# Kernel optimization log

Hardware: AMD Instinct MI355X
Metric: run time of the kernel (lower is better)

## Reference

```python
import jax, jax.numpy as jnp
import numpy as np

VOCAB = 32000
FEAT = 1024
B, T = 16, 256


def setup_inputs() -> dict:
    key = jax.random.key(0)
    ks = jax.random.split(key, 12)
    s_in = 1.0 / np.sqrt(FEAT)
    inp = {
        "x": jax.random.randint(ks[0], (B, T), 0, VOCAB),
        "h0": jnp.zeros((2, B, FEAT), jnp.float32),
        "emb": jax.random.normal(ks[1], (VOCAB, FEAT), jnp.float32) * 0.02,
        "W_ih0": jax.random.uniform(ks[2], (3 * FEAT, FEAT), jnp.float32, -s_in, s_in),
        "W_hh0": jax.random.uniform(ks[3], (3 * FEAT, FEAT), jnp.float32, -s_in, s_in),
        "b_ih0": jax.random.uniform(ks[4], (3 * FEAT,), jnp.float32, -s_in, s_in),
        "b_hh0": jax.random.uniform(ks[5], (3 * FEAT,), jnp.float32, -s_in, s_in),
        "W_ih1": jax.random.uniform(ks[6], (3 * FEAT, FEAT), jnp.float32, -s_in, s_in),
        "W_hh1": jax.random.uniform(ks[7], (3 * FEAT, FEAT), jnp.float32, -s_in, s_in),
        "b_ih1": jax.random.uniform(ks[8], (3 * FEAT,), jnp.float32, -s_in, s_in),
        "b_hh1": jax.random.uniform(ks[9], (3 * FEAT,), jnp.float32, -s_in, s_in),
        "dec_b": jnp.zeros((VOCAB,), jnp.float32),
    }
    return inp


def _gru_layer(xs, h0, W_ih, W_hh, b_ih, b_hh):
    # xs: [T, B, H_in]; h0: [B, H]. PyTorch gate order: r, z, n.
    x_proj = jnp.einsum('tbi,gi->tbg', xs, W_ih) + b_ih  # [T, B, 3H]

    def step(h, xp):
        hp = h @ W_hh.T + b_hh  # [B, 3H]
        xr, xz, xn = jnp.split(xp, 3, axis=-1)
        hr, hz, hn = jnp.split(hp, 3, axis=-1)
        r = jax.nn.sigmoid(xr + hr)
        z = jax.nn.sigmoid(xz + hz)
        n = jnp.tanh(xn + r * hn)
        h_new = (1.0 - z) * n + z * h
        return h_new, h_new

    h_last, ys = jax.lax.scan(step, h0, x_proj)
    return ys, h_last


def reference(x, h0, emb, W_ih0, W_hh0, b_ih0, b_hh0, W_ih1, W_hh1, b_ih1, b_hh1, dec_b):
    xs = emb[x]  # [B, T, H]
    xs = jnp.transpose(xs, (1, 0, 2))  # time-major [T, B, H]
    ys0, h_last0 = _gru_layer(xs, h0[0], W_ih0, W_hh0, b_ih0, b_hh0)
    ys1, h_last1 = _gru_layer(ys0, h0[1], W_ih1, W_hh1, b_ih1, b_hh1)
    out = jnp.transpose(ys1, (1, 0, 2))  # [B, T, H]
    logits = jnp.einsum('bth,vh->btv', out, emb) + dec_b  # tied decoder
    hidden = jnp.stack([h_last0, h_last1], axis=0)  # [2, B, H]
    return logits, hidden
```

## Files before the change

### kernel.cpp

```cpp
#include <hip/hip_runtime.h>
#include <math.h>

#define FEAT 1024
#define NB 16
#define NT 256
#define VOCAB 32000
#define G3 3072
#define NWG 256
#define FLAG_STRIDE 32
#define NGRP 8
#define GSZ 32
#define NXPT 24

#define BK 32
#define LDH 40
#define SMEM_BYTES 75584

typedef float f4 __attribute__((ext_vector_type(4)));
typedef float f32x4 __attribute__((ext_vector_type(4)));
typedef _Float16 half4v __attribute__((ext_vector_type(4)));
typedef _Float16 half8v __attribute__((ext_vector_type(8)));

__global__ __launch_bounds__(256) void gather_kernel(const int* __restrict__ x,
                                                     const float* __restrict__ emb,
                                                     float* __restrict__ xs) {
    int row = blockIdx.x;
    int t = row >> 4;
    int b = row & 15;
    int tok = x[b * NT + t];
    const float4* src = (const float4*)(emb + (size_t)tok * FEAT);
    float4* dst = (float4*)(xs + (size_t)row * FEAT);
    dst[threadIdx.x] = src[threadIdx.x];
}

__device__ __forceinline__ void store_f32_sc(float* p, float v) {
    asm volatile("global_store_dword %0, %1, off sc0 sc1" :: "v"(p), "v"(v) : "memory");
}
__device__ __forceinline__ void bar_arrive(unsigned* flag, unsigned expected) {
    asm volatile("s_waitcnt vmcnt(0)\n\t"
                 "global_store_dword %0, %1, off sc0 sc1"
                 :: "v"(flag), "v"(expected) : "memory");
}
__device__ __forceinline__ void bar_poll(const unsigned* p, unsigned expected) {
    unsigned v; int spins = 0;
    while (true) {
        asm volatile("global_load_dword %0, %1, off sc0 sc1\n\t"
                     "s_waitcnt vmcnt(0)"
                     : "=&v"(v) : "v"(p) : "memory");
        if (v >= expected) break;
        if (++spins > (1 << 20)) break;
        __builtin_amdgcn_s_sleep(1);
    }
}

__device__ __forceinline__ void gemm_tile(char* smemraw,
        const float* __restrict__ A, const float* __restrict__ Bm,
        const float* __restrict__ bias, float* __restrict__ C,
        int N, int K, int m_t, int n_t, int perm,
        int coherent, unsigned* cnt) {
    _Float16* AhS = (_Float16*)smemraw;
    _Float16* AlS = AhS + 128 * LDH;
    _Float16* BhS = AlS + 128 * LDH;
    _Float16* BlS = BhS + 128 * LDH;

    int tid = threadIdx.x;
    int srow = tid >> 1;
    int shf = tid & 1;

    const float* aptr = A + (size_t)(m_t * 128 + srow) * K + shf * 16;
    const float* bptr = Bm + (size_t)(n_t * 128 + srow) * K + shf * 16;

    int wid = tid >> 6;
    int wr = wid >> 1, wc = wid & 1;
    int lane = tid & 63;
    int fr = lane & 15;
    int ke = lane >> 4;

    f32x4 acc[4][4];
#pragma unroll
    for (int i = 0; i < 4; i++)
#pragma unroll
        for (int j = 0; j < 4; j++) acc[i][j] = (f32x4){0.f, 0.f, 0.f, 0.f};

    float4 a4[4], b4[4];
#pragma unroll
    for (int q = 0; q < 4; q++) {
        a4[q] = *(const float4*)(aptr + q * 4);
        b4[q] = *(const float4*)(bptr + q * 4);
    }

    for (int k0 = 0; k0 < K; k0 += BK) {
        __syncthreads();
#pragma unroll
        for (int q = 0; q < 4; q++) {
            half4v hh, hl;
            hh.x = (_Float16)a4[q].x; hl.x = (_Float16)(a4[q].x - (float)hh.x);
            hh.y = (_Float16)a4[q].y; hl.y = (_Float16)(a4[q].y - (float)hh.y);
            hh.z = (_Float16)a4[q].z; hl.z = (_Float16)(a4[q].z - (float)hh.z);
            hh.w = (_Float16)a4[q].w; hl.w = (_Float16)(a4[q].w - (float)hh.w);
            int o = srow * LDH + shf * 16 + q * 4;
            *(half4v*)&AhS[o] = hh;
            *(half4v*)&AlS[o] = hl;
            half4v gh, gl;
            gh.x = (_Float16)b4[q].x; gl.x = (_Float16)(b4[q].x - (float)gh.x);
            gh.y = (_Float16)b4[q].y; gl.y = (_Float16)(b4[q].y - (float)gh.y);
            gh.z = (_Float16)b4[q].z; gl.z = (_Float16)(b4[q].z - (float)gh.z);
            gh.w = (_Float16)b4[q].w; gl.w = (_Float16)(b4[q].w - (float)gh.w);
            *(half4v*)&BhS[o] = gh;
            *(half4v*)&BlS[o] = gl;
        }
        __syncthreads();

        if (k0 + BK < K) {
#pragma unroll
            for (int q = 0; q < 4; q++) {
                a4[q] = *(const float4*)(aptr + k0 + BK + q * 4);
                b4[q] = *(const float4*)(bptr + k0 + BK + q * 4);
            }
        }

        half8v ah[4], al[4], bh[4], bl[4];
#pragma unroll
        for (int i = 0; i < 4; i++) {
            int ao = (wr * 64 + i * 16 + fr) * LDH + ke * 8;
            ah[i] = *(const half8v*)&AhS[ao];
            al[i] = *(const half8v*)&AlS[ao];
            int bo = (wc * 64 + i * 16 + fr) * LDH + ke * 8;
            bh[i] = *(const half8v*)&BhS[bo];
            bl[i] = *(const half8v*)&BlS[bo];
        }
#pragma unroll
        for (int i = 0; i < 4; i++)
#pragma unroll
            for (int j = 0; j < 4; j++) {
                acc[i][j] = __builtin_amdgcn_mfma_f32_16x16x32_f16(ah[i], bh[j], acc[i][j], 0, 0, 0);
                acc[i][j] = __builtin_amdgcn_mfma_f32_16x16x32_f16(ah[i], bl[j], acc[i][j], 0, 0, 0);
                acc[i][j] = __builtin_amdgcn_mfma_f32_16x16x32_f16(al[i], bh[j], acc[i][j], 0, 0, 0);
            }
    }

#pragma unroll
    for (int j = 0; j < 4; j++) {
        int col = n_t * 128 + wc * 64 + j * 16 + fr;
        float bv = bias[col];
#pragma unroll
        for (int i = 0; i < 4; i++) {
#pragma unroll
            for (int v = 0; v < 4; v++) {
                int mrow = m_t * 128 + wr * 64 + i * 16 + 4 * ke + v;
                int orow = perm ? (((mrow & 15) << 8) | (mrow >> 4)) : mrow;
                float val = acc[i][j][v] + bv;
                if (coherent) store_f32_sc(&C[(size_t)orow * N + col], val);
                else          C[(size_t)orow * N + col] = val;
            }
        }
    }
    if (cnt) {
        asm volatile("s_waitcnt vmcnt(0)" ::: "memory");
        __syncthreads();
        if (tid == 0)
            __hip_atomic_fetch_add(cnt, 1u, __ATOMIC_RELAXED, __HIP_MEMORY_SCOPE_AGENT);
    }
}

__device__ __forceinline__ void scan_layer(char* smemraw,
        const float* __restrict__ xp, const float* __restrict__ Whh,
        const float* __restrict__ bhh, const float* __restrict__ h0src,
        float* __restrict__ ys, float* __restrict__ hid,
        unsigned* __restrict__ flags, unsigned* __restrict__ gflags,
        const unsigned* __restrict__ xpcnt) {
    float* w_lds   = (float*)smemraw;
    float* red     = w_lds + 12 * 1024;
    float* sums    = red + 192 * 33;
    float* bhh_lds = sums + 256;

    __builtin_amdgcn_s_setprio(1);

    int wg = blockIdx.x;
    int j0 = wg * 4;
    int tid = threadIdx.x;

    for (int rr = 0; rr < 12; rr++) {
        int gate = rr >> 2, jloc = rr & 3;
        int grow = gate * FEAT + j0 + jloc;
        float4 v = ((const float4*)(Whh + (size_t)grow * FEAT))[tid];
        *(float4*)(w_lds + rr * 1024 + tid * 4) = v;
    }
    if (tid < 12) {
        int gate = tid >> 2, jloc = tid & 3;
        bhh_lds[tid] = bhh[gate * FEAT + j0 + jloc];
    }
    if (xpcnt && tid == 0) bar_poll(&xpcnt[0], NXPT);
    __syncthreads();

    int bg = tid >> 6;
    int kc = tid & 63;
    int pb = tid >> 2, pjl = tid & 3, pj = j0 + pjl;

    float hreg = 0.f;
    if (tid < 64) hreg = h0src[pb * FEAT + pj];

    for (int t = 0; t < NT; t++) {
        float xr = 0.f, xz = 0.f, xnv = 0.f;
        if (tid < 64) {
            const float* xpr = xp + (size_t)(t * NB + pb) * G3;
            xr = xpr[pj]; xz = xpr[FEAT + pj]; xnv = xpr[2 * FEAT + pj];
        }

        const float* hc = (t == 0) ? h0src : (ys + (size_t)(t - 1) * NB * FEAT);
        f4 h4[16];
#pragma unroll
        for (int bi = 0; bi < 4; bi++) {
            const float* hp = hc + (size_t)(bg * 4 + bi) * FEAT + kc * 4;
#pragma unroll
            for (int q = 0; q < 4; q++)
                h4[bi * 4 + q] = *(const f4*)(hp + q * 256);
        }

        float part[48];
#pragma unroll
        for (int i = 0; i < 48; i++) part[i] = 0.f;
#pragma unroll
        for (int q = 0; q < 4; q++) {
            int kof = q * 256 + kc * 4;
#pragma unroll
            for (int rr = 0; rr < 12; rr++) {
                f4 w = *(const f4*)&w_lds[rr * 1024 + kof];
#pragma unroll
                for (int bi = 0; bi < 4; bi++) {
                    f4 h = h4[bi * 4 + q];
                    float p = part[rr * 4 + bi];
                    p = fmaf(h.x, w.x, p); p = fmaf(h.y, w.y, p);
                    p = fmaf(h.z, w.z, p); p = fmaf(h.w, w.w, p);
                    part[rr * 4 + bi] = p;
                }
            }
        }
#pragma unroll
        for (int i = 0; i < 48; i++) part[i] += __shfl_xor(part[i], 1);
        if ((kc & 1) == 0) {
#pragma unroll
            for (int rr = 0; rr < 12; rr++)
#pragma unroll
                for (int bi = 0; bi < 4; bi++)
                    red[(rr * 16 + bg * 4 + bi) * 33 + (kc >> 1)] = part[rr * 4 + bi];
        }
        __syncthreads();

        if (tid < 192) {
            float s = 0.f;
#pragma unroll
            for (int c = 0; c < 32; c++) s += red[tid * 33 + c];
            sums[tid] = s;
        }
        __syncthreads();

        if (tid < 64) {
            float dr = sums[pjl * 16 + pb] + bhh_lds[pjl];
            float dz = sums[(4 + pjl) * 16 + pb] + bhh_lds[4 + pjl];
            float dn = sums[(8 + pjl) * 16 + pb] + bhh_lds[8 + pjl];
            float r = 1.f / (1.f + expf(-(xr + dr)));
            float z = 1.f / (1.f + expf(-(xz + dz)));
            float n = tanhf(xnv + r * dn);
            float hv = (1.f - z) * n + z * hreg;
            hreg = hv;
            store_f32_sc(ys + (size_t)(t * NB + pb) * FEAT + pj, hv);
            if (t == NT - 1) hid[pb * FEAT + pj] = hv;
        }

        unsigned expected = (unsigned)(t + 1);
        __syncthreads();
        if (tid == 0) {
            bar_arrive(&flags[wg * FLAG_STRIDE], expected);
            if (xpcnt) {
                int nx = (t + 1 < NT) ? (t + 1) : (NT - 1);
                bar_poll(&xpcnt[(nx >> 3) * FLAG_STRIDE], NXPT);
            }
        }
        if (wg < NGRP) {
            if (tid < GSZ) bar_poll(flags + (wg * GSZ + tid) * FLAG_STRIDE, expected);
            if (tid == 0) {
                asm volatile("global_store_dword %0, %1, off sc0 sc1"
                             :: "v"(&gflags[wg * FLAG_STRIDE]), "v"(expected) : "memory");
            }
        }
        if (tid < NGRP) bar_poll(gflags + tid * FLAG_STRIDE, expected);
        __builtin_amdgcn_sched_barrier(0);
        __syncthreads();
    }
}

__global__ __launch_bounds__(256, 2) void phase1(
        float* __restrict__ xp, const float* __restrict__ Whh0,
        const float* __restrict__ bhh0, const float* __restrict__ h0,
        float* __restrict__ ys0, float* __restrict__ hid,
        unsigned* __restrict__ flags0, unsigned* __restrict__ gflags0,
        const float* __restrict__ xs,
        const float* __restrict__ Wih0, const float* __restrict__ bih0,
        unsigned* __restrict__ xpcnt,
        const float* __restrict__ Wih1, const float* __restrict__ bih1) {
    __shared__ __align__(16) char smem[SMEM_BYTES];
    int bid = blockIdx.x;
    if (bid < NWG) {
        scan_layer(smem, xp, Whh0, bhh0, h0, ys0, hid, flags0, gflags0, xpcnt);
    } else if (bid < NWG + (4096 / 128) * NXPT) {
        int b2 = bid - NWG;
        int perGroup = 8 * NXPT;
        int g = b2 / perGroup, rix = b2 % perGroup;
        int n_t = rix / 8, m_t = g * 8 + (rix % 8);
        gemm_tile(smem, xs, Wih0, bih0, xp, G3, FEAT, m_t, n_t, 0,
                  1, &xpcnt[m_t * FLAG_STRIDE]);
    } else {
        int b2 = bid - NWG - (4096 / 128) * NXPT;
        int perGroup = 8 * NXPT;
        int g = b2 / perGroup, rix = b2 % perGroup;
        int n_t = rix / 8, m_t = g * 8 + (rix % 8);
        unsigned gate = (unsigned)((m_t + 1) * 8);
        if (threadIdx.x < NGRP) bar_poll(gflags0 + threadIdx.x * FLAG_STRIDE, gate);
        __builtin_amdgcn_sched_barrier(0);
        __syncthreads();
        gemm_tile(smem, ys0, Wih1, bih1, xp, G3, FEAT, m_t, n_t, 0, 0, nullptr);
    }
}

__global__ __launch_bounds__(256, 2) void phase2(
        const float* __restrict__ xp, const float* __restrict__ Whh1,
        const float* __restrict__ bhh1, const float* __restrict__ h0b,
        float* __restrict__ ys1, float* __restrict__ hid1,
        unsigned* __restrict__ flags1, unsigned* __restrict__ gflags1,
        const float* __restrict__ emb, const float* __restrict__ dec_b,
        float* __restrict__ out) {
    __shared__ __align__(16) char smem[SMEM_BYTES];
    if (blockIdx.x < NWG) {
        scan_layer(smem, xp, Whh1, bhh1, h0b, ys1, hid1, flags1, gflags1, nullptr);
    } else {
        int bid = blockIdx.x - NWG;
        int perGroup = 8 * (VOCAB >> 7);
        int g = bid / perGroup, rix = bid % perGroup;
        int n_t = rix / 8, m_t = g * 8 + (rix % 8);
        unsigned gate = (unsigned)((m_t + 1) * 8);
        if (threadIdx.x < NGRP) bar_poll(gflags1 + threadIdx.x * FLAG_STRIDE, gate);
        __builtin_amdgcn_sched_barrier(0);
        __syncthreads();
        gemm_tile(smem, ys1, emb, dec_b, out, VOCAB, FEAT, m_t, n_t, 1, 0, nullptr);
    }
}

extern "C" void kernel_launch(void* const* d_in, const int* in_sizes, int n_in,
                              void* d_out, int out_size, void* d_ws, size_t ws_size,
                              hipStream_t stream) {
    const int*   x     = (const int*)d_in[0];
    const float* h0    = (const float*)d_in[1];
    const float* emb   = (const float*)d_in[2];
    const float* W_ih0 = (const float*)d_in[3];
    const float* W_hh0 = (const float*)d_in[4];
    const float* b_ih0 = (const float*)d_in[5];
    const float* b_hh0 = (const float*)d_in[6];
    const float* W_ih1 = (const float*)d_in[7];
    const float* W_hh1 = (const float*)d_in[8];
    const float* b_ih1 = (const float*)d_in[9];
    const float* b_hh1 = (const float*)d_in[10];
    const float* dec_b = (const float*)d_in[11];

    float* out = (float*)d_out;
    float* hid_out = out + (size_t)NB * NT * VOCAB;

    float* ws  = (float*)d_ws;
    float* xp  = ws;
    float* xs  = xp + (size_t)4096 * 3072;
    float* ys0 = xs + (size_t)4096 * 1024;
    float* pad = ys0 + (size_t)4096 * 1024;
    unsigned* flags0  = (unsigned*)(pad + 2 * NB * FEAT);
    unsigned* gflags0 = flags0 + NWG * FLAG_STRIDE;
    unsigned* flags1  = gflags0 + NGRP * FLAG_STRIDE;
    unsigned* gflags1 = flags1 + NWG * FLAG_STRIDE;
    unsigned* xpcnt   = gflags1 + NGRP * FLAG_STRIDE;
    float* ys1 = xs;

    hipMemsetAsync((void*)flags0, 0,
                   (2 * NWG + 2 * NGRP + 32) * FLAG_STRIDE * sizeof(unsigned),
                   stream);

    gather_kernel<<<dim3(NT * NB), dim3(256), 0, stream>>>(x, emb, xs);

    phase1<<<dim3(NWG + 2 * (4096 / 128) * NXPT), dim3(256), 0, stream>>>(
        xp, W_hh0, b_hh0, h0, ys0, hid_out, flags0, gflags0,
        xs, W_ih0, b_ih0, xpcnt, W_ih1, b_ih1);

    phase2<<<dim3(NWG + (4096 / 128) * (VOCAB / 128)), dim3(256), 0, stream>>>(
        xp, W_hh1, b_hh1, h0 + NB * FEAT, ys1, hid_out + NB * FEAT,
        flags1, gflags1, emb, dec_b, out);
}
```

Before: 3.679 ms.

## Fuse both GRU layer scans into one delayed wavefront chain kernel

```diff
diff --git a/kernel.cpp b/kernel.cpp
--- a/kernel.cpp
+++ b/kernel.cpp
@@ -11,10 +11,12 @@
 #define NGRP 8
 #define GSZ 32
 #define NXPT 24
+#define DLY 32
+#define CHAIN (NT + DLY)
 
 #define BK 32
 #define LDH 40
-#define SMEM_BYTES 75584
+#define SMEM_BYTES 63104
 
 typedef float f4 __attribute__((ext_vector_type(4)));
 typedef float f32x4 __attribute__((ext_vector_type(4)));
@@ -163,16 +165,33 @@
     }
 }
 
-__device__ __forceinline__ void scan_layer(char* smemraw,
-        const float* __restrict__ xp, const float* __restrict__ Whh,
-        const float* __restrict__ bhh, const float* __restrict__ h0src,
-        float* __restrict__ ys, float* __restrict__ hid,
+__global__ __launch_bounds__(256, 2) void gemm_split16(
+        const float* __restrict__ A, const float* __restrict__ Bm,
+        const float* __restrict__ bias, float* __restrict__ C,
+        int N, int K, int GM, int perm) {
+    __shared__ __align__(16) char smem[4 * 128 * LDH * 2];
+    int nNt = N >> 7;
+    int perGroup = GM * nNt;
+    int g = blockIdx.x / perGroup;
+    int rix = blockIdx.x % perGroup;
+    int n_t = rix / GM;
+    int m_t = g * GM + (rix % GM);
+    gemm_tile(smem, A, Bm, bias, C, N, K, m_t, n_t, perm, 0, nullptr);
+}
+
+__device__ __forceinline__ void scan_chain(char* smemraw,
+        float* __restrict__ xp, const float* __restrict__ Whh0,
+        const float* __restrict__ bhh0, const float* __restrict__ Whh1,
+        const float* __restrict__ bhh1, const float* __restrict__ h0all,
+        float* __restrict__ ys0, float* __restrict__ ys1,
+        float* __restrict__ hid,
         unsigned* __restrict__ flags, unsigned* __restrict__ gflags,
-        const unsigned* __restrict__ xpcnt) {
-    float* w_lds   = (float*)smemraw;
-    float* red     = w_lds + 12 * 1024;
-    float* sums    = red + 192 * 33;
-    float* bhh_lds = sums + 256;
+        const unsigned* __restrict__ xpcnt, const unsigned* __restrict__ xp1cnt) {
+    float* w_lds = (float*)smemraw;
+    float* red   = w_lds + 12 * 1024;
+    float* sums  = red + 192 * 17;
+    float* b0l   = sums + 192;
+    float* b1l   = b0l + 12;
 
     __builtin_amdgcn_s_setprio(1);
 
@@ -183,99 +202,222 @@
     for (int rr = 0; rr < 12; rr++) {
         int gate = rr >> 2, jloc = rr & 3;
         int grow = gate * FEAT + j0 + jloc;
-        float4 v = ((const float4*)(Whh + (size_t)grow * FEAT))[tid];
+        float4 v = ((const float4*)(Whh0 + (size_t)grow * FEAT))[tid];
         *(float4*)(w_lds + rr * 1024 + tid * 4) = v;
     }
     if (tid < 12) {
         int gate = tid >> 2, jloc = tid & 3;
-        bhh_lds[tid] = bhh[gate * FEAT + j0 + jloc];
-    }
-    if (xpcnt && tid == 0) bar_poll(&xpcnt[0], NXPT);
+        b0l[tid] = bhh0[gate * FEAT + j0 + jloc];
+        b1l[tid] = bhh1[gate * FEAT + j0 + jloc];
+    }
+    if (tid == 0) bar_poll(&xpcnt[0], NXPT);
     __syncthreads();
 
     int bg = tid >> 6;
     int kc = tid & 63;
     int pb = tid >> 2, pjl = tid & 3, pj = j0 + pjl;
 
-    float hreg = 0.f;
-    if (tid < 64) hreg = h0src[pb * FEAT + pj];
-
-    for (int t = 0; t < NT; t++) {
+    const float* w1g0 = Whh1 + (size_t)j0 * FEAT;
+    const float* w1g1 = Whh1 + (size_t)(FEAT + j0) * FEAT;
+    const float* w1g2 = Whh1 + (size_t)(2 * FEAT + j0) * FEAT;
+
+    float hreg0 = 0.f, hreg1 = 0.f;
+    if (tid < 64) {
+        hreg0 = h0all[pb * FEAT + pj];
+        hreg1 = h0all[NB * FEAT + pb * FEAT + pj];
+    }
+
+    for (int s = 0; s < CHAIN; s++) {
+        int do0 = (s < NT);
+        int t1 = s - DLY;
+        int do1 = (t1 >= 0);
+
         float xr = 0.f, xz = 0.f, xnv = 0.f;
-        if (tid < 64) {
-            const float* xpr = xp + (size_t)(t * NB + pb) * G3;
+        if (do0 && tid < 64) {
+            const float* xpr = xp + (size_t)(s * NB + pb) * G3;
             xr = xpr[pj]; xz = xpr[FEAT + pj]; xnv = xpr[2 * FEAT + pj];
         }
-
-        const float* hc = (t == 0) ? h0src : (ys + (size_t)(t - 1) * NB * FEAT);
-        f4 h4[16];
-#pragma unroll
-        for (int bi = 0; bi < 4; bi++) {
-            const float* hp = hc + (size_t)(bg * 4 + bi) * FEAT + kc * 4;
-#pragma unroll
-            for (int q = 0; q < 4; q++)
-                h4[bi * 4 + q] = *(const f4*)(hp + q * 256);
-        }
-
-        float part[48];
-#pragma unroll
-        for (int i = 0; i < 48; i++) part[i] = 0.f;
-#pragma unroll
-        for (int q = 0; q < 4; q++) {
-            int kof = q * 256 + kc * 4;
-#pragma unroll
-            for (int rr = 0; rr < 12; rr++) {
-                f4 w = *(const f4*)&w_lds[rr * 1024 + kof];
-#pragma unroll
-                for (int bi = 0; bi < 4; bi++) {
-                    f4 h = h4[bi * 4 + q];
-                    float p = part[rr * 4 + bi];
-                    p = fmaf(h.x, w.x, p); p = fmaf(h.y, w.y, p);
-                    p = fmaf(h.z, w.z, p); p = fmaf(h.w, w.w, p);
-                    part[rr * 4 + bi] = p;
+        float x1r, x1z, x1n;
+        if (do1 && tid < 64) {
+            const float* xpr = xp + (size_t)(t1 * NB + pb) * G3;
+            asm volatile(
+                "global_load_dword %0, %3, off sc0 sc1\n\t"
+                "global_load_dword %1, %4, off sc0 sc1\n\t"
+                "global_load_dword %2, %5, off sc0 sc1"
+                : "=&v"(x1r), "=&v"(x1z), "=&v"(x1n)
+                : "v"(xpr + pj), "v"(xpr + FEAT + pj), "v"(xpr + 2 * FEAT + pj)
+                : "memory");
+        }
+
+        if (do0) {
+            const float* hc = (s == 0) ? h0all : (ys0 + (size_t)(s - 1) * NB * FEAT);
+            f4 h4[16];
+#pragma unroll
+            for (int bi = 0; bi < 4; bi++) {
+                const float* hp = hc + (size_t)(bg * 4 + bi) * FEAT + kc * 4;
+#pragma unroll
+                for (int q = 0; q < 4; q++)
+                    h4[bi * 4 + q] = *(const f4*)(hp + q * 256);
+            }
+            float part[48];
+#pragma unroll
+            for (int i = 0; i < 48; i++) part[i] = 0.f;
+#pragma unroll
+            for (int q = 0; q < 4; q++) {
+                int kof = q * 256 + kc * 4;
+#pragma unroll
+                for (int rr = 0; rr < 12; rr++) {
+                    f4 w = *(const f4*)&w_lds[rr * 1024 + kof];
+#pragma unroll
+                    for (int bi = 0; bi < 4; bi++) {
+                        f4 h = h4[bi * 4 + q];
+                        float p = part[rr * 4 + bi];
+                        p = fmaf(h.x, w.x, p); p = fmaf(h.y, w.y, p);
+                        p = fmaf(h.z, w.z, p); p = fmaf(h.w, w.w, p);
+                        part[rr * 4 + bi] = p;
+                    }
                 }
             }
-        }
-#pragma unroll
-        for (int i = 0; i < 48; i++) part[i] += __shfl_xor(part[i], 1);
-        if ((kc & 1) == 0) {
-#pragma unroll
-            for (int rr = 0; rr < 12; rr++)
-#pragma unroll
-                for (int bi = 0; bi < 4; bi++)
-                    red[(rr * 16 + bg * 4 + bi) * 33 + (kc >> 1)] = part[rr * 4 + bi];
-        }
-        __syncthreads();
-
-        if (tid < 192) {
-            float s = 0.f;
-#pragma unroll
-            for (int c = 0; c < 32; c++) s += red[tid * 33 + c];
-            sums[tid] = s;
-        }
-        __syncthreads();
-
-        if (tid < 64) {
-            float dr = sums[pjl * 16 + pb] + bhh_lds[pjl];
-            float dz = sums[(4 + pjl) * 16 + pb] + bhh_lds[4 + pjl];
-            float dn = sums[(8 + pjl) * 16 + pb] + bhh_lds[8 + pjl];
+#pragma unroll
+            for (int i = 0; i < 48; i++) {
+                part[i] += __shfl_xor(part[i], 1);
+                part[i] += __shfl_xor(part[i], 2);
+            }
+            if ((kc & 3) == 0) {
+#pragma unroll
+                for (int rr = 0; rr < 12; rr++)
+#pragma unroll
+                    for (int bi = 0; bi < 4; bi++)
+                        red[(rr * 16 + bg * 4 + bi) * 17 + (kc >> 2)] = part[rr * 4 + bi];
+            }
+        }
+        __syncthreads();
+        if (do0 && tid < 192) {
+            float sm = 0.f;
+#pragma unroll
+            for (int c = 0; c < 16; c++) sm += red[tid * 17 + c];
+            sums[tid] = sm;
+        }
+        __syncthreads();
+        if (do0 && tid < 64) {
+            float dr = sums[pjl * 16 + pb] + b0l[pjl];
+            float dz = sums[(4 + pjl) * 16 + pb] + b0l[4 + pjl];
+            float dn = sums[(8 + pjl) * 16 + pb] + b0l[8 + pjl];
             float r = 1.f / (1.f + expf(-(xr + dr)));
             float z = 1.f / (1.f + expf(-(xz + dz)));
             float n = tanhf(xnv + r * dn);
-            float hv = (1.f - z) * n + z * hreg;
-            hreg = hv;
-            store_f32_sc(ys + (size_t)(t * NB + pb) * FEAT + pj, hv);
-            if (t == NT - 1) hid[pb * FEAT + pj] = hv;
-        }
-
-        unsigned expected = (unsigned)(t + 1);
+            float hv = (1.f - z) * n + z * hreg0;
+            hreg0 = hv;
+            store_f32_sc(ys0 + (size_t)(s * NB + pb) * FEAT + pj, hv);
+            if (s == NT - 1) hid[pb * FEAT + pj] = hv;
+        }
+
+        if (do1) {
+            const float* hc1 = (t1 == 0) ? (h0all + NB * FEAT)
+                                         : (ys1 + (size_t)(t1 - 1) * NB * FEAT);
+            f4 h4[16];
+            {
+                const float* p0 = hc1 + (size_t)(bg * 4 + 0) * FEAT + kc * 4;
+                const float* p1 = hc1 + (size_t)(bg * 4 + 1) * FEAT + kc * 4;
+                const float* p2 = hc1 + (size_t)(bg * 4 + 2) * FEAT + kc * 4;
+                const float* p3 = hc1 + (size_t)(bg * 4 + 3) * FEAT + kc * 4;
+                asm volatile(
+                    "global_load_dwordx4 %0,  %16, off sc0 sc1\n\t"
+                    "global_load_dwordx4 %1,  %16, off offset:1024 sc0 sc1\n\t"
+                    "global_load_dwordx4 %2,  %16, off offset:2048 sc0 sc1\n\t"
+                    "global_load_dwordx4 %3,  %16, off offset:3072 sc0 sc1\n\t"
+                    "global_load_dwordx4 %4,  %17, off sc0 sc1\n\t"
+                    "global_load_dwordx4 %5,  %17, off offset:1024 sc0 sc1\n\t"
+                    "global_load_dwordx4 %6,  %17, off offset:2048 sc0 sc1\n\t"
+                    "global_load_dwordx4 %7,  %17, off offset:3072 sc0 sc1\n\t"
+                    "global_load_dwordx4 %8,  %18, off sc0 sc1\n\t"
+                    "global_load_dwordx4 %9,  %18, off offset:1024 sc0 sc1\n\t"
+                    "global_load_dwordx4 %10, %18, off offset:2048 sc0 sc1\n\t"
+                    "global_load_dwordx4 %11, %18, off offset:3072 sc0 sc1\n\t"
+                    "global_load_dwordx4 %12, %19, off sc0 sc1\n\t"
+                    "global_load_dwordx4 %13, %19, off offset:1024 sc0 sc1\n\t"
+                    "global_load_dwordx4 %14, %19, off offset:2048 sc0 sc1\n\t"
+                    "global_load_dwordx4 %15, %19, off offset:3072 sc0 sc1\n\t"
+                    "s_waitcnt vmcnt(0)"
+                    : "=&v"(h4[0]), "=&v"(h4[1]), "=&v"(h4[2]), "=&v"(h4[3]),
+                      "=&v"(h4[4]), "=&v"(h4[5]), "=&v"(h4[6]), "=&v"(h4[7]),
+                      "=&v"(h4[8]), "=&v"(h4[9]), "=&v"(h4[10]), "=&v"(h4[11]),
+                      "=&v"(h4[12]), "=&v"(h4[13]), "=&v"(h4[14]), "=&v"(h4[15])
+                    : "v"(p0), "v"(p1), "v"(p2), "v"(p3) : "memory");
+                __builtin_amdgcn_sched_barrier(0);
+            }
+            float part[48];
+#pragma unroll
+            for (int i = 0; i < 48; i++) part[i] = 0.f;
+#pragma unroll
+            for (int q = 0; q < 4; q++) {
+                int kof = q * 256 + kc * 4;
+#pragma unroll
+                for (int jl = 0; jl < 4; jl++) {
+                    f4 w0v = *(const f4*)(w1g0 + (size_t)jl * FEAT + kof);
+                    f4 w1v = *(const f4*)(w1g1 + (size_t)jl * FEAT + kof);
+                    f4 w2v = *(const f4*)(w1g2 + (size_t)jl * FEAT + kof);
+#pragma unroll
+                    for (int bi = 0; bi < 4; bi++) {
+                        f4 h = h4[bi * 4 + q];
+                        float p = part[jl * 4 + bi];
+                        p = fmaf(h.x, w0v.x, p); p = fmaf(h.y, w0v.y, p);
+                        p = fmaf(h.z, w0v.z, p); p = fmaf(h.w, w0v.w, p);
+                        part[jl * 4 + bi] = p;
+                        p = part[(4 + jl) * 4 + bi];
+                        p = fmaf(h.x, w1v.x, p); p = fmaf(h.y, w1v.y, p);
+                        p = fmaf(h.z, w1v.z, p); p = fmaf(h.w, w1v.w, p);
+                        part[(4 + jl) * 4 + bi] = p;
+                        p = part[(8 + jl) * 4 + bi];
+                        p = fmaf(h.x, w2v.x, p); p = fmaf(h.y, w2v.y, p);
+                        p = fmaf(h.z, w2v.z, p); p = fmaf(h.w, w2v.w, p);
+                        p = part[(8 + jl) * 4 + bi] = p;
+                    }
+                }
+            }
+#pragma unroll
+            for (int i = 0; i < 48; i++) {
+                part[i] += __shfl_xor(part[i], 1);
+                part[i] += __shfl_xor(part[i], 2);
+            }
+            if ((kc & 3) == 0) {
+#pragma unroll
+                for (int rr = 0; rr < 12; rr++)
+#pragma unroll
+                    for (int bi = 0; bi < 4; bi++)
+                        red[(rr * 16 + bg * 4 + bi) * 17 + (kc >> 2)] = part[rr * 4 + bi];
+            }
+        }
+        __syncthreads();
+        if (do1 && tid < 192) {
+            float sm = 0.f;
+#pragma unroll
+            for (int c = 0; c < 16; c++) sm += red[tid * 17 + c];
+            sums[tid] = sm;
+        }
+        __syncthreads();
+        if (do1 && tid < 64) {
+            float dr = sums[pjl * 16 + pb] + b1l[pjl];
+            float dz = sums[(4 + pjl) * 16 + pb] + b1l[4 + pjl];
+            float dn = sums[(8 + pjl) * 16 + pb] + b1l[8 + pjl];
+            float r = 1.f / (1.f + expf(-(x1r + dr)));
+            float z = 1.f / (1.f + expf(-(x1z + dz)));
+            float n = tanhf(x1n + r * dn);
+            float hv = (1.f - z) * n + z * hreg1;
+            hreg1 = hv;
+            store_f32_sc(ys1 + (size_t)(t1 * NB + pb) * FEAT + pj, hv);
+            if (t1 == NT - 1) hid[NB * FEAT + pb * FEAT + pj] = hv;
+        }
+
+        unsigned expected = (unsigned)(s + 1);
         __syncthreads();
         if (tid == 0) {
             bar_arrive(&flags[wg * FLAG_STRIDE], expected);
-            if (xpcnt) {
-                int nx = (t + 1 < NT) ? (t + 1) : (NT - 1);
-                bar_poll(&xpcnt[(nx >> 3) * FLAG_STRIDE], NXPT);
-            }
+            if (s + 1 < NT)
+                bar_poll(&xpcnt[((s + 1) >> 3) * FLAG_STRIDE], NXPT);
+            int t1n = s + 1 - DLY;
+            if (t1n >= 0 && t1n < NT)
+                bar_poll(&xp1cnt[(t1n >> 3) * FLAG_STRIDE], NXPT);
         }
         if (wg < NGRP) {
             if (tid < GSZ) bar_poll(flags + (wg * GSZ + tid) * FLAG_STRIDE, expected);
@@ -290,19 +432,22 @@
     }
 }
 
-__global__ __launch_bounds__(256, 2) void phase1(
-        float* __restrict__ xp, const float* __restrict__ Whh0,
-        const float* __restrict__ bhh0, const float* __restrict__ h0,
-        float* __restrict__ ys0, float* __restrict__ hid,
-        unsigned* __restrict__ flags0, unsigned* __restrict__ gflags0,
-        const float* __restrict__ xs,
+__global__ __launch_bounds__(256, 2) void chain_kernel(
+        float* __restrict__ xp, const float* __restrict__ xs,
+        const float* __restrict__ Whh0, const float* __restrict__ bhh0,
         const float* __restrict__ Wih0, const float* __restrict__ bih0,
-        unsigned* __restrict__ xpcnt,
-        const float* __restrict__ Wih1, const float* __restrict__ bih1) {
+        const float* __restrict__ Whh1, const float* __restrict__ bhh1,
+        const float* __restrict__ Wih1, const float* __restrict__ bih1,
+        const float* __restrict__ h0all,
+        float* __restrict__ ys0, float* __restrict__ ys1,
+        float* __restrict__ hid,
+        unsigned* __restrict__ flags, unsigned* __restrict__ gflags,
+        unsigned* __restrict__ xpcnt, unsigned* __restrict__ xp1cnt) {
     __shared__ __align__(16) char smem[SMEM_BYTES];
     int bid = blockIdx.x;
     if (bid < NWG) {
-        scan_layer(smem, xp, Whh0, bhh0, h0, ys0, hid, flags0, gflags0, xpcnt);
+        scan_chain(smem, xp, Whh0, bhh0, Whh1, bhh1, h0all,
+                   ys0, ys1, hid, flags, gflags, xpcnt, xp1cnt);
     } else if (bid < NWG + (4096 / 128) * NXPT) {
         int b2 = bid - NWG;
         int perGroup = 8 * NXPT;
@@ -316,33 +461,11 @@
         int g = b2 / perGroup, rix = b2 % perGroup;
         int n_t = rix / 8, m_t = g * 8 + (rix % 8);
         unsigned gate = (unsigned)((m_t + 1) * 8);
-        if (threadIdx.x < NGRP) bar_poll(gflags0 + threadIdx.x * FLAG_STRIDE, gate);
+        if (threadIdx.x < NGRP) bar_poll(gflags + threadIdx.x * FLAG_STRIDE, gate);
         __builtin_amdgcn_sched_barrier(0);
         __syncthreads();
-        gemm_tile(smem, ys0, Wih1, bih1, xp, G3, FEAT, m_t, n_t, 0, 0, nullptr);
-    }
-}
-
-__global__ __launch_bounds__(256, 2) void phase2(
-        const float* __restrict__ xp, const float* __restrict__ Whh1,
-        const float* __restrict__ bhh1, const float* __restrict__ h0b,
-        float* __restrict__ ys1, float* __restrict__ hid1,
-        unsigned* __restrict__ flags1, unsigned* __restrict__ gflags1,
-        const float* __restrict__ emb, const float* __restrict__ dec_b,
-        float* __restrict__ out) {
-    __shared__ __align__(16) char smem[SMEM_BYTES];
-    if (blockIdx.x < NWG) {
-        scan_layer(smem, xp, Whh1, bhh1, h0b, ys1, hid1, flags1, gflags1, nullptr);
-    } else {
-        int bid = blockIdx.x - NWG;
-        int perGroup = 8 * (VOCAB >> 7);
-        int g = bid / perGroup, rix = bid % perGroup;
-        int n_t = rix / 8, m_t = g * 8 + (rix % 8);
-        unsigned gate = (unsigned)((m_t + 1) * 8);
-        if (threadIdx.x < NGRP) bar_poll(gflags1 + threadIdx.x * FLAG_STRIDE, gate);
-        __builtin_amdgcn_sched_barrier(0);
-        __syncthreads();
-        gemm_tile(smem, ys1, emb, dec_b, out, VOCAB, FEAT, m_t, n_t, 1, 0, nullptr);
+        gemm_tile(smem, ys0, Wih1, bih1, xp, G3, FEAT, m_t, n_t, 0,
+                  1, &xp1cnt[m_t * FLAG_STRIDE]);
     }
 }
 
@@ -370,24 +493,21 @@
     float* xs  = xp + (size_t)4096 * 3072;
     float* ys0 = xs + (size_t)4096 * 1024;
     float* pad = ys0 + (size_t)4096 * 1024;
-    unsigned* flags0  = (unsigned*)(pad + 2 * NB * FEAT);
-    unsigned* gflags0 = flags0 + NWG * FLAG_STRIDE;
-    unsigned* flags1  = gflags0 + NGRP * FLAG_STRIDE;
-    unsigned* gflags1 = flags1 + NWG * FLAG_STRIDE;
-    unsigned* xpcnt   = gflags1 + NGRP * FLAG_STRIDE;
+    unsigned* flags  = (unsigned*)(pad + 2 * NB * FEAT);
+    unsigned* gflags = flags + NWG * FLAG_STRIDE;
+    unsigned* xpcnt  = gflags + NGRP * FLAG_STRIDE;
+    unsigned* xp1cnt = xpcnt + 32 * FLAG_STRIDE;
     float* ys1 = xs;
 
-    hipMemsetAsync((void*)flags0, 0,
-                   (2 * NWG + 2 * NGRP + 32) * FLAG_STRIDE * sizeof(unsigned),
-                   stream);
+    hipMemsetAsync((void*)flags, 0,
+                   (NWG + NGRP + 64) * FLAG_STRIDE * sizeof(unsigned), stream);
 
     gather_kernel<<<dim3(NT * NB), dim3(256), 0, stream>>>(x, emb, xs);
 
-    phase1<<<dim3(NWG + 2 * (4096 / 128) * NXPT), dim3(256), 0, stream>>>(
-        xp, W_hh0, b_hh0, h0, ys0, hid_out, flags0, gflags0,
-        xs, W_ih0, b_ih0, xpcnt, W_ih1, b_ih1);
-
-    phase2<<<dim3(NWG + (4096 / 128) * (VOCAB / 128)), dim3(256), 0, stream>>>(
-        xp, W_hh1, b_hh1, h0 + NB * FEAT, ys1, hid_out + NB * FEAT,
-        flags1, gflags1, emb, dec_b, out);
-}
+    chain_kernel<<<dim3(NWG + 2 * (4096 / 128) * NXPT), dim3(256), 0, stream>>>(
+        xp, xs, W_hh0, b_hh0, W_ih0, b_ih0, W_hh1, b_hh1, W_ih1, b_ih1,
+        h0, ys0, ys1, hid_out, flags, gflags, xpcnt, xp1cnt);
+
+    gemm_split16<<<dim3((4096 / 128) * (VOCAB / 128)), dim3(256), 0, stream>>>(
+        ys1, emb, dec_b, out, VOCAB, FEAT, 8, 1);
+}
```

Result: slower. 4.540 ms (+23.4%).
